# Kernel optimization log

Hardware: AMD Instinct MI355X
Metric: run time of the kernel (lower is better)

## Reference

```python
import jax, jax.numpy as jnp
import numpy as np

H = 1024
EM = 512
I_SIZE = 32000
O_SIZE = 32000
ENC_LEN = 2048
DEC_LEN = 2048
START_IDX = 1


def setup_inputs() -> dict:
    key = jax.random.key(0)
    ks = jax.random.split(key, 16)
    s = 1.0 / np.sqrt(H)
    u = lambda k, shape: jax.random.uniform(k, shape, jnp.float32, -s, s)
    return {
        "e1": jax.random.randint(ks[0], (ENC_LEN,), 0, I_SIZE),
        "gt": jax.random.randint(ks[1], (DEC_LEN,), 0, O_SIZE),
        "emb_i": jax.random.normal(ks[2], (I_SIZE, EM), jnp.float32),
        "emb_o": jax.random.normal(ks[3], (O_SIZE, EM), jnp.float32),
        "enc_Wih": u(ks[4], (4 * H, EM)),
        "enc_Whh": u(ks[5], (4 * H, H)),
        "enc_bih": u(ks[6], (4 * H,)),
        "enc_bhh": u(ks[7], (4 * H,)),
        "dec_Wih": u(ks[8], (4 * H, EM)),
        "dec_Whh": u(ks[9], (4 * H, H)),
        "dec_bih": u(ks[10], (4 * H,)),
        "dec_bhh": u(ks[11], (4 * H,)),
        "outW": u(ks[12], (O_SIZE, H)),
        "outb": u(ks[13], (O_SIZE,)),
    }


def _lstm_scan(embs, h0, c0, Wih, Whh, bih, bhh):
    """Run an LSTMCell over embs [T, EM]; returns (h_T, c_T, all h [T, H])."""
    # Precompute input contributions for all steps in one GEMM: [T, 4H]
    x_gates = embs @ Wih.T + (bih + bhh)

    def step(carry, xg):
        h, c = carry
        g = xg + h @ Whh.T                      # [4H]
        i, f, gg, o = jnp.split(g, 4)
        c = jax.nn.sigmoid(f) * c + jax.nn.sigmoid(i) * jnp.tanh(gg)
        h = jax.nn.sigmoid(o) * jnp.tanh(c)
        return (h, c), h

    (hT, cT), hs = jax.lax.scan(step, (h0, c0), x_gates)
    return hT, cT, hs


def reference(e1, gt, emb_i, emb_o, enc_Wih, enc_Whh, enc_bih, enc_bhh,
              dec_Wih, dec_Whh, dec_bih, dec_bhh, outW, outb):
    # ----- encode: final CELL state is returned (original: out, c = h; return c)
    enc_embs = emb_i[e1]                                   # [ENC_LEN, EM]
    zeros = jnp.zeros((H,), enc_embs.dtype)
    _, enc_c, _ = _lstm_scan(enc_embs, zeros, zeros,
                             enc_Wih, enc_Whh, enc_bih, enc_bhh)

    # ----- decode with teacher forcing: h = (enc, enc)
    dec_in = jnp.concatenate([jnp.array([START_IDX], gt.dtype), gt[:-1]])
    dec_embs = emb_o[dec_in]                               # [DEC_LEN, EM]
    _, _, hs = _lstm_scan(dec_embs, enc_c, enc_c,
                          dec_Wih, dec_Whh, dec_bih, dec_bhh)

    logits = hs @ outW.T + outb                            # [DEC_LEN, O_SIZE]
    return logits
```

## Files before the change

### kernel.cpp

```cpp
#include <hip/hip_runtime.h>

#define H 1024
#define EM 512
#define TSTEPS 2048
#define OSZ 32000
#define FOURH 4096
#define NWG 128

typedef __attribute__((ext_vector_type(8))) short short8;
typedef __attribute__((ext_vector_type(4))) float f32x4;

__device__ __forceinline__ unsigned short f2bf(float f) {
  union { float f; unsigned int u; } x; x.f = f;
  unsigned int r = x.u + 0x7FFFu + ((x.u >> 16) & 1u);
  return (unsigned short)(r >> 16);
}
__device__ __forceinline__ unsigned int pk2(float lo, float hi) {
  return (unsigned int)f2bf(lo) | ((unsigned int)f2bf(hi) << 16);
}
__device__ __forceinline__ float fast_sigm(float x) {
  return __builtin_amdgcn_rcpf(1.0f + __expf(-x));
}
__device__ __forceinline__ float fast_tanh(float x) {
  return 1.0f - 2.0f * __builtin_amdgcn_rcpf(1.0f + __expf(2.0f * x));
}

#define DPP_ADD(x, ctrl) \
  ((x) + __int_as_float(__builtin_amdgcn_update_dpp( \
       0, __float_as_int(x), (ctrl), 0xf, 0xf, true)))

__global__ void gather_k(const int* __restrict__ e1, const int* __restrict__ gt,
                         const float* __restrict__ emb_i, const float* __restrict__ emb_o,
                         float* __restrict__ enc_e, float* __restrict__ dec_e) {
  int row = blockIdx.x;
  int t4 = threadIdx.x * 4;
  if (blockIdx.y == 0) {
    int idx = e1[row];
    *(float4*)&enc_e[(size_t)row * EM + t4] = *(const float4*)&emb_i[(size_t)idx * EM + t4];
  } else {
    int idx = (row == 0) ? 1 : gt[row - 1];
    *(float4*)&dec_e[(size_t)row * EM + t4] = *(const float4*)&emb_o[(size_t)idx * EM + t4];
  }
}

#define LDT 40
__global__ __launch_bounds__(256) void gemm_bt(
    const float* __restrict__ A, const float* __restrict__ B,
    const float* __restrict__ bias1, const float* __restrict__ bias2,
    float* __restrict__ C, int M, int N, int K) {
  __shared__ __align__(16) unsigned short aL[64 * LDT];
  __shared__ __align__(16) unsigned short bL[64 * LDT];
  int tid = threadIdx.x;
  int n0 = blockIdx.x * 64, m0 = blockIdx.y * 64;
  int wv = tid >> 6, l = tid & 63;
  int wm = (wv >> 1) * 32, wn = (wv & 1) * 32;
  int col = l & 15, quad = l >> 4;
  f32x4 acc[2][2];
  acc[0][0] = (f32x4){0,0,0,0}; acc[0][1] = (f32x4){0,0,0,0};
  acc[1][0] = (f32x4){0,0,0,0}; acc[1][1] = (f32x4){0,0,0,0};

  int r = tid >> 2, c8 = (tid & 3) * 8;
  const float* ap = A + (size_t)(m0 + r) * K + c8;
  const float* bp = B + (size_t)(n0 + r) * K + c8;

  for (int k0 = 0; k0 < K; k0 += 32) {
    float4 a0 = *(const float4*)(ap + k0);
    float4 a1 = *(const float4*)(ap + k0 + 4);
    float4 b0 = *(const float4*)(bp + k0);
    float4 b1 = *(const float4*)(bp + k0 + 4);
    uint4 apk, bpk;
    apk.x = pk2(a0.x, a0.y); apk.y = pk2(a0.z, a0.w);
    apk.z = pk2(a1.x, a1.y); apk.w = pk2(a1.z, a1.w);
    bpk.x = pk2(b0.x, b0.y); bpk.y = pk2(b0.z, b0.w);
    bpk.z = pk2(b1.x, b1.y); bpk.w = pk2(b1.z, b1.w);
    *(uint4*)&aL[r * LDT + c8] = apk;
    *(uint4*)&bL[r * LDT + c8] = bpk;
    __syncthreads();

    short8 af0 = *(const short8*)&aL[(wm + col) * LDT + quad * 8];
    short8 af1 = *(const short8*)&aL[(wm + 16 + col) * LDT + quad * 8];
    short8 bf0 = *(const short8*)&bL[(wn + col) * LDT + quad * 8];
    short8 bf1 = *(const short8*)&bL[(wn + 16 + col) * LDT + quad * 8];
    acc[0][0] = __builtin_amdgcn_mfma_f32_16x16x32_bf16(af0, bf0, acc[0][0], 0, 0, 0);
    acc[0][1] = __builtin_amdgcn_mfma_f32_16x16x32_bf16(af0, bf1, acc[0][1], 0, 0, 0);
    acc[1][0] = __builtin_amdgcn_mfma_f32_16x16x32_bf16(af1, bf0, acc[1][0], 0, 0, 0);
    acc[1][1] = __builtin_amdgcn_mfma_f32_16x16x32_bf16(af1, bf1, acc[1][1], 0, 0, 0);
    __syncthreads();
  }

  #pragma unroll
  for (int j = 0; j < 2; ++j) {
    int n = n0 + wn + j * 16 + col;
    float b = (bias1 ? bias1[n] : 0.0f) + (bias2 ? bias2[n] : 0.0f);
    #pragma unroll
    for (int i = 0; i < 2; ++i) {
      #pragma unroll
      for (int rg = 0; rg < 4; ++rg) {
        int m = m0 + wm + i * 16 + quad * 4 + rg;
        C[(size_t)m * N + n] = acc[i][j][rg] + b;
      }
    }
  }
}

__global__ __launch_bounds__(256, 1) void lstm_k(
    const float* __restrict__ xg, const float* __restrict__ Whh,
    const float* __restrict__ h0c0, unsigned long long* __restrict__ pair,
    float* __restrict__ hs, float* __restrict__ c_out) {
  __shared__ __align__(16) float h_lds[H];
  __shared__ float gate_lds[32];
  __shared__ float c_lds[8];
  int tid = threadIdx.x;
  int wg = blockIdx.x;
  int w = tid >> 6, l = tid & 63;
  int a = l >> 4, q = l & 15;
  int q4 = q * 4;
  int hbase = wg * 8;
  int rowA = w * H + hbase + a;
  int rowB = rowA + 4;

  const float* wpA = Whh + (size_t)rowA * H + q4;
  const float* wpB = Whh + (size_t)rowB * H + q4;
#define LOADW(i) \
  f32x4 wA##i = *(const f32x4*)(wpA + (i) * 64); \
  f32x4 wB##i = *(const f32x4*)(wpB + (i) * 64);
  LOADW(0)  LOADW(1)  LOADW(2)  LOADW(3)
  LOADW(4)  LOADW(5)  LOADW(6)  LOADW(7)
  LOADW(8)  LOADW(9)  LOADW(10) LOADW(11)
  LOADW(12) LOADW(13) LOADW(14) LOADW(15)
#undef LOADW
  asm volatile("" : "+v"(wA0), "+v"(wA1), "+v"(wA2), "+v"(wA3),
                    "+v"(wA4), "+v"(wA5), "+v"(wA6), "+v"(wA7));
  asm volatile("" : "+v"(wA8), "+v"(wA9), "+v"(wA10), "+v"(wA11),
                    "+v"(wA12), "+v"(wA13), "+v"(wA14), "+v"(wA15));
  asm volatile("" : "+v"(wB0), "+v"(wB1), "+v"(wB2), "+v"(wB3),
                    "+v"(wB4), "+v"(wB5), "+v"(wB6), "+v"(wB7));
  asm volatile("" : "+v"(wB8), "+v"(wB9), "+v"(wB10), "+v"(wB11),
                    "+v"(wB12), "+v"(wB13), "+v"(wB14), "+v"(wB15));

  for (int i = tid; i < H; i += 256) h_lds[i] = h0c0 ? h0c0[i] : 0.0f;
  if (tid < 8) c_lds[tid] = h0c0 ? h0c0[hbase + tid] : 0.0f;
  __syncthreads();

  const float* xgp = xg + w * H + hbase + a + (q == 1 ? 4 : 0);
  float xgv_next = (q < 2) ? xgp[0] : 0.0f;

  for (int t = 0; t < TSTEPS; ++t) {
    float xgv = xgv_next;
    if (q < 2 && t + 1 < TSTEPS) xgv_next = xgp[(size_t)(t + 1) * FOURH];

    float sA0 = 0, sA1 = 0, sB0 = 0, sB1 = 0;
#define FMA(i) { \
    f32x4 hv = *(const f32x4*)&h_lds[(i) * 64 + q4]; \
    sA0 += wA##i.x * hv.x + wA##i.y * hv.y; \
    sA1 += wA##i.z * hv.z + wA##i.w * hv.w; \
    sB0 += wB##i.x * hv.x + wB##i.y * hv.y; \
    sB1 += wB##i.z * hv.z + wB##i.w * hv.w; }
    FMA(0)  FMA(1)  FMA(2)  FMA(3)
    FMA(4)  FMA(5)  FMA(6)  FMA(7)
    FMA(8)  FMA(9)  FMA(10) FMA(11)
    FMA(12) FMA(13) FMA(14) FMA(15)
#undef FMA
    float accA = sA0 + sA1, accB = sB0 + sB1;
    accA = DPP_ADD(accA, 0xB1);  accB = DPP_ADD(accB, 0xB1);
    accA = DPP_ADD(accA, 0x4E);  accB = DPP_ADD(accB, 0x4E);
    accA = DPP_ADD(accA, 0x124); accB = DPP_ADD(accB, 0x124);
    accA = DPP_ADD(accA, 0x128); accB = DPP_ADD(accB, 0x128);

    float gv = ((q == 0) ? accA : accB) + xgv;
    float act = (w == 2) ? fast_tanh(gv) : fast_sigm(gv);
    if (q == 0)      gate_lds[w * 8 + a]     = act;
    else if (q == 1) gate_lds[w * 8 + a + 4] = act;
    __syncthreads();

    if (tid < 8) {
      int j = tid;
      float gi = gate_lds[j], gf = gate_lds[8 + j], gg = gate_lds[16 + j], go = gate_lds[24 + j];
      float c = gf * c_lds[j] + gi * gg;
      float h = go * fast_tanh(c);
      c_lds[j] = c;
      unsigned long long pkd = (unsigned long long)__float_as_uint(h) |
                               ((unsigned long long)(unsigned int)(t + 1) << 32);
      __hip_atomic_store(&pair[(size_t)t * H + hbase + j], pkd,
                         __ATOMIC_RELAXED, __HIP_MEMORY_SCOPE_AGENT);
      if (hs) hs[(size_t)t * H + hbase + j] = h;
    }

    if (t + 1 < TSTEPS) {
      int base = tid * 4;
      const unsigned long long* src = pair + (size_t)t * H + base;
      unsigned int want = (unsigned int)(t + 1);
      float v[4]; unsigned int done = 0;
      while (done != 0xFu) {
        #pragma unroll
        for (int i = 0; i < 4; ++i) {
          if (!(done & (1u << i))) {
            unsigned long long p = __hip_atomic_load(&src[i], __ATOMIC_RELAXED,
                                                     __HIP_MEMORY_SCOPE_AGENT);
            if ((unsigned int)(p >> 32) == want) {
              v[i] = __uint_as_float((unsigned int)p);
              done |= (1u << i);
            }
          }
        }
      }
      h_lds[base] = v[0]; h_lds[base + 1] = v[1];
      h_lds[base + 2] = v[2]; h_lds[base + 3] = v[3];
    }
    __syncthreads();
  }
  if (c_out && tid < 8) c_out[hbase + tid] = c_lds[tid];
}

extern "C" void kernel_launch(void* const* d_in, const int* in_sizes, int n_in,
                              void* d_out, int out_size, void* d_ws, size_t ws_size,
                              hipStream_t stream) {
  const int*   e1      = (const int*)d_in[0];
  const int*   gt      = (const int*)d_in[1];
  const float* emb_i   = (const float*)d_in[2];
  const float* emb_o   = (const float*)d_in[3];
  const float* enc_Wih = (const float*)d_in[4];
  const float* enc_Whh = (const float*)d_in[5];
  const float* enc_bih = (const float*)d_in[6];
  const float* enc_bhh = (const float*)d_in[7];
  const float* dec_Wih = (const float*)d_in[8];
  const float* dec_Whh = (const float*)d_in[9];
  const float* dec_bih = (const float*)d_in[10];
  const float* dec_bhh = (const float*)d_in[11];
  const float* outW    = (const float*)d_in[12];
  const float* outb    = (const float*)d_in[13];
  float* out = (float*)d_out;

  char* ws = (char*)d_ws;
  size_t off = 0;
  float* enc_embs = (float*)(ws + off); off += (size_t)TSTEPS * EM * 4;
  float* dec_embs = (float*)(ws + off); off += (size_t)TSTEPS * EM * 4;
  float* xg_enc   = (float*)(ws + off); off += (size_t)TSTEPS * FOURH * 4;
  float* xg_dec   = (float*)(ws + off); off += (size_t)TSTEPS * FOURH * 4;
  unsigned long long* pair_enc = (unsigned long long*)(ws + off); off += (size_t)TSTEPS * H * 8;
  unsigned long long* pair_dec = (unsigned long long*)(ws + off); off += (size_t)TSTEPS * H * 8;
  float* enc_c = (float*)(ws + off);    off += (size_t)H * 4;
  float* hs    = (float*)(ws + off);    off += (size_t)TSTEPS * H * 4;

  gather_k<<<dim3(TSTEPS, 2), 128, 0, stream>>>(e1, gt, emb_i, emb_o, enc_embs, dec_embs);
  gemm_bt<<<dim3(FOURH / 64, TSTEPS / 64), 256, 0, stream>>>(
      enc_embs, enc_Wih, enc_bih, enc_bhh, xg_enc, TSTEPS, FOURH, EM);
  lstm_k<<<NWG, 256, 0, stream>>>(xg_enc, enc_Whh, nullptr, pair_enc, nullptr, enc_c);
  gemm_bt<<<dim3(FOURH / 64, TSTEPS / 64), 256, 0, stream>>>(
      dec_embs, dec_Wih, dec_bih, dec_bhh, xg_dec, TSTEPS, FOURH, EM);
  lstm_k<<<NWG, 256, 0, stream>>>(xg_dec, dec_Whh, enc_c, pair_dec, hs, nullptr);
  gemm_bt<<<dim3(OSZ / 64, TSTEPS / 64), 256, 0, stream>>>(
      hs, outW, outb, nullptr, out, TSTEPS, OSZ, H);
}
```

Baseline: 10.92 ms.

## Compute LSTM cell per wave via shuffles and double-buffer padded h exchange

```diff
diff --git a/kernel.cpp b/kernel.cpp
--- a/kernel.cpp
+++ b/kernel.cpp
@@ -6,6 +6,7 @@
 #define OSZ 32000
 #define FOURH 4096
 #define NWG 128
+#define PSTRIDE 16
 
 typedef __attribute__((ext_vector_type(8))) short short8;
 typedef __attribute__((ext_vector_type(4))) float f32x4;
@@ -108,16 +109,15 @@
     const float* __restrict__ h0c0, unsigned long long* __restrict__ pair,
     float* __restrict__ hs, float* __restrict__ c_out) {
   __shared__ __align__(16) float h_lds[H];
-  __shared__ float gate_lds[32];
-  __shared__ float c_lds[8];
   int tid = threadIdx.x;
   int wg = blockIdx.x;
   int w = tid >> 6, l = tid & 63;
   int a = l >> 4, q = l & 15;
   int q4 = q * 4;
   int hbase = wg * 8;
-  int rowA = w * H + hbase + a;
-  int rowB = rowA + 4;
+  int hA = hbase + 2 * w;
+  int rowA = a * H + hA;
+  int rowB = rowA + 1;
 
   const float* wpA = Whh + (size_t)rowA * H + q4;
   const float* wpB = Whh + (size_t)rowB * H + q4;
@@ -139,10 +139,11 @@
                     "+v"(wB12), "+v"(wB13), "+v"(wB14), "+v"(wB15));
 
   for (int i = tid; i < H; i += 256) h_lds[i] = h0c0 ? h0c0[i] : 0.0f;
-  if (tid < 8) c_lds[tid] = h0c0 ? h0c0[hbase + tid] : 0.0f;
+  float cA = h0c0 ? h0c0[hA] : 0.0f;
+  float cB = h0c0 ? h0c0[hA + 1] : 0.0f;
   __syncthreads();
 
-  const float* xgp = xg + w * H + hbase + a + (q == 1 ? 4 : 0);
+  const float* xgp = xg + rowA + (q == 1 ? 1 : 0);
   float xgv_next = (q < 2) ? xgp[0] : 0.0f;
 
   for (int t = 0; t < TSTEPS; ++t) {
@@ -161,42 +162,61 @@
     FMA(8)  FMA(9)  FMA(10) FMA(11)
     FMA(12) FMA(13) FMA(14) FMA(15)
 #undef FMA
-    float accA = sA0 + sA1, accB = sB0 + sB1;
+    float accA = sA0 + sA1 + ((q == 0) ? xgv : 0.0f);
+    float accB = sB0 + sB1 + ((q == 1) ? xgv : 0.0f);
     accA = DPP_ADD(accA, 0xB1);  accB = DPP_ADD(accB, 0xB1);
     accA = DPP_ADD(accA, 0x4E);  accB = DPP_ADD(accB, 0x4E);
     accA = DPP_ADD(accA, 0x124); accB = DPP_ADD(accB, 0x124);
     accA = DPP_ADD(accA, 0x128); accB = DPP_ADD(accB, 0x128);
 
-    float gv = ((q == 0) ? accA : accB) + xgv;
-    float act = (w == 2) ? fast_tanh(gv) : fast_sigm(gv);
-    if (q == 0)      gate_lds[w * 8 + a]     = act;
-    else if (q == 1) gate_lds[w * 8 + a + 4] = act;
-    __syncthreads();
-
-    if (tid < 8) {
-      int j = tid;
-      float gi = gate_lds[j], gf = gate_lds[8 + j], gg = gate_lds[16 + j], go = gate_lds[24 + j];
-      float c = gf * c_lds[j] + gi * gg;
-      float h = go * fast_tanh(c);
-      c_lds[j] = c;
-      unsigned long long pkd = (unsigned long long)__float_as_uint(h) |
+    float kk = (a == 2) ? 2.0f : -1.0f;
+    float rA = __builtin_amdgcn_rcpf(1.0f + __expf(kk * accA));
+    float rB = __builtin_amdgcn_rcpf(1.0f + __expf(kk * accB));
+    float actA = (a == 2) ? 1.0f - 2.0f * rA : rA;
+    float actB = (a == 2) ? 1.0f - 2.0f * rB : rB;
+
+    float fA1 = __shfl_xor(actA, 16);
+    float fB1 = __shfl_xor(actB, 16);
+    float fA2 = __shfl_xor(actA, 32);
+    float fB2 = __shfl_xor(actB, 32);
+    float fA3 = __shfl_xor(fA1, 32);
+    float fB3 = __shfl_xor(fB1, 32);
+    float gi_A = (a == 0) ? actA : (a == 1) ? fA1 : (a == 2) ? fA2 : fA3;
+    float gf_A = (a == 1) ? actA : (a == 0) ? fA1 : (a == 3) ? fA2 : fA3;
+    float gg_A = (a == 2) ? actA : (a == 3) ? fA1 : (a == 0) ? fA2 : fA3;
+    float go_A = (a == 3) ? actA : (a == 2) ? fA1 : (a == 1) ? fA2 : fA3;
+    float gi_B = (a == 0) ? actB : (a == 1) ? fB1 : (a == 2) ? fB2 : fB3;
+    float gf_B = (a == 1) ? actB : (a == 0) ? fB1 : (a == 3) ? fB2 : fB3;
+    float gg_B = (a == 2) ? actB : (a == 3) ? fB1 : (a == 0) ? fB2 : fB3;
+    float go_B = (a == 3) ? actB : (a == 2) ? fB1 : (a == 1) ? fB2 : fB3;
+
+    cA = gf_A * cA + gi_A * gg_A;
+    cB = gf_B * cB + gi_B * gg_B;
+    float hAv = go_A * fast_tanh(cA);
+    float hBv = go_B * fast_tanh(cB);
+
+    if (l < 2) {
+      float hv = (l == 0) ? hAv : hBv;
+      int hidx = hA + l;
+      unsigned long long pkd = (unsigned long long)__float_as_uint(hv) |
                                ((unsigned long long)(unsigned int)(t + 1) << 32);
-      __hip_atomic_store(&pair[(size_t)t * H + hbase + j], pkd,
+      __hip_atomic_store(&pair[(size_t)((t & 1) * H + hidx) * PSTRIDE], pkd,
                          __ATOMIC_RELAXED, __HIP_MEMORY_SCOPE_AGENT);
-      if (hs) hs[(size_t)t * H + hbase + j] = h;
+      if (hs) hs[(size_t)t * H + hidx] = hv;
     }
 
     if (t + 1 < TSTEPS) {
       int base = tid * 4;
-      const unsigned long long* src = pair + (size_t)t * H + base;
+      const unsigned long long* src = pair + (size_t)(t & 1) * H * PSTRIDE;
       unsigned int want = (unsigned int)(t + 1);
       float v[4]; unsigned int done = 0;
       while (done != 0xFu) {
         #pragma unroll
         for (int i = 0; i < 4; ++i) {
           if (!(done & (1u << i))) {
-            unsigned long long p = __hip_atomic_load(&src[i], __ATOMIC_RELAXED,
-                                                     __HIP_MEMORY_SCOPE_AGENT);
+            unsigned long long p = __hip_atomic_load(
+                &src[(size_t)(base + i) * PSTRIDE], __ATOMIC_RELAXED,
+                __HIP_MEMORY_SCOPE_AGENT);
             if ((unsigned int)(p >> 32) == want) {
               v[i] = __uint_as_float((unsigned int)p);
               done |= (1u << i);
@@ -209,7 +229,7 @@
     }
     __syncthreads();
   }
-  if (c_out && tid < 8) c_out[hbase + tid] = c_lds[tid];
+  if (c_out && l < 2) c_out[hA + l] = (l == 0) ? cA : cB;
 }
 
 extern "C" void kernel_launch(void* const* d_in, const int* in_sizes, int n_in,
@@ -237,8 +257,10 @@
   float* dec_embs = (float*)(ws + off); off += (size_t)TSTEPS * EM * 4;
   float* xg_enc   = (float*)(ws + off); off += (size_t)TSTEPS * FOURH * 4;
   float* xg_dec   = (float*)(ws + off); off += (size_t)TSTEPS * FOURH * 4;
-  unsigned long long* pair_enc = (unsigned long long*)(ws + off); off += (size_t)TSTEPS * H * 8;
-  unsigned long long* pair_dec = (unsigned long long*)(ws + off); off += (size_t)TSTEPS * H * 8;
+  unsigned long long* pair_enc = (unsigned long long*)(ws + off);
+  off += (size_t)2 * H * PSTRIDE * 8;
+  unsigned long long* pair_dec = (unsigned long long*)(ws + off);
+  off += (size_t)2 * H * PSTRIDE * 8;
   float* enc_c = (float*)(ws + off);    off += (size_t)H * 4;
   float* hs    = (float*)(ws + off);    off += (size_t)TSTEPS * H * 4;
 
```

After: 15.00 ms. +37.4%, slower.
